# Performance work log

Measured on AMD Instinct MI355X. Metric: run time of the kernel, lower is better.

The kernel has to match this reference:

```python
import jax, jax.numpy as jnp
import numpy as np
from jax import lax

N = 2048          # batch_size*2 (two views)
DIM_IN = 1024     # stub encoder input width
DIM_FEAT = 2048
DIM = 128
C = 1000          # num_classes
Q = 8             # queue_size_per_cls
K_POS = 4         # select_num_pos
K_NEG = 1024      # select_num_neg
EPS = 1e-5


def setup_inputs() -> dict:
    key = jax.random.key(0)
    ks = jax.random.split(key, 12)
    img = jax.random.normal(ks[0], (N, DIM_IN), dtype=jnp.float32)
    labels = jax.random.randint(ks[1], (N,), 0, C)
    # buffers
    ql = jax.random.normal(ks[2], (DIM, Q * C), dtype=jnp.float32)
    queue_list = ql / jnp.linalg.norm(ql, axis=0, keepdims=True)
    queue_ptr = jnp.zeros((C,), dtype=jnp.int32)
    pos_index = jnp.asarray(np.arange(Q * C).reshape(C, Q))
    cols = np.arange(Q * (C - 1))
    # skip class-i block: indices >= Q*i shift up by Q
    neg_index = jnp.asarray(cols[None, :] + Q * ((cols[None, :] // Q) >= np.arange(C)[:, None]))
    # params (stub encoder + mlp head + classifier)
    s = 0.02
    enc_W = s * jax.random.normal(ks[3], (DIM_IN, DIM_FEAT), dtype=jnp.float32)
    enc_b = jnp.zeros((DIM_FEAT,), dtype=jnp.float32)
    mlp_W1 = s * jax.random.normal(ks[4], (DIM_FEAT, DIM_FEAT), dtype=jnp.float32)
    mlp_b1 = jnp.zeros((DIM_FEAT,), dtype=jnp.float32)
    bn_gamma = jnp.ones((DIM_FEAT,), dtype=jnp.float32)
    bn_beta = jnp.zeros((DIM_FEAT,), dtype=jnp.float32)
    mlp_W2 = s * jax.random.normal(ks[5], (DIM_FEAT, DIM), dtype=jnp.float32)
    mlp_b2 = jnp.zeros((DIM,), dtype=jnp.float32)
    lin_W = s * jax.random.normal(ks[6], (DIM_FEAT, C), dtype=jnp.float32)
    lin_b = jnp.zeros((C,), dtype=jnp.float32)
    return dict(img=img, labels=labels, queue_list=queue_list, queue_ptr=queue_ptr,
                pos_index=pos_index, neg_index=neg_index,
                enc_W=enc_W, enc_b=enc_b, mlp_W1=mlp_W1, mlp_b1=mlp_b1,
                bn_gamma=bn_gamma, bn_beta=bn_beta, mlp_W2=mlp_W2, mlp_b2=mlp_b2,
                lin_W=lin_W, lin_b=lin_b)


def _offdiag_idx(n):
    # idx[i,j] = j + (j >= i): gather columns of an [n,n] matrix skipping the diagonal
    cols = jnp.arange(n - 1)
    return cols[None, :] + (cols[None, :] >= jnp.arange(n)[:, None]).astype(cols.dtype)


def reference(img, labels, queue_list, queue_ptr, pos_index, neg_index,
              enc_W, enc_b, mlp_W1, mlp_b1, bn_gamma, bn_beta,
              mlp_W2, mlp_b2, lin_W, lin_b):
    # encoder (stub) -> mid_feat
    mid = img @ enc_W + enc_b                                  # [N, DIM_FEAT]
    # mlp: Linear -> BatchNorm1d (training stats) -> ReLU -> Linear
    h = mid @ mlp_W1 + mlp_b1
    mu = jnp.mean(h, axis=0)
    var = jnp.var(h, axis=0)
    h = (h - mu) * lax.rsqrt(var + EPS) * bn_gamma + bn_beta
    h = jax.nn.relu(h)
    feat = h @ mlp_W2 + mlp_b2
    feat = feat / jnp.linalg.norm(feat, axis=1, keepdims=True)  # [N, DIM]
    logit_cls = mid @ lin_W + lin_b                             # [N, C]

    # queue similarities (queue is detached in the original)
    ql = lax.stop_gradient(queue_list)
    sim_q = feat @ ql                                           # [N, Q*C]
    sim_pos = jnp.take_along_axis(sim_q, pos_index[labels], axis=1)   # [N, Q]
    sim_neg = jnp.take_along_axis(sim_q, neg_index[labels], axis=1)   # [N, Q*(C-1)]
    pos_sel = -lax.top_k(-sim_pos, K_POS)[0]     # hardest (smallest) positives
    neg_sel = lax.top_k(sim_neg, K_NEG)[0]       # hardest (largest) negatives

    # in-batch similarities with diagonal removed
    sim_b = feat @ feat.T                                       # [N, N]
    off = _offdiag_idx(sim_b.shape[0])
    sim_b_off = jnp.take_along_axis(sim_b, off, axis=1)         # [N, N-1]
    sim_con = jnp.concatenate([sim_b_off, pos_sel, neg_sel], axis=1)

    lab_b = (labels[:, None] == labels[None, :]).astype(jnp.float32)
    lab_off = jnp.take_along_axis(lab_b, off, axis=1)
    labels_con = jnp.concatenate([lab_off, jnp.ones_like(pos_sel), jnp.zeros_like(neg_sel)], axis=1)

    # dequeue/enqueue: sequential per-sample scatter into per-class circular buffer
    feat_k = lax.stop_gradient(feat[: feat.shape[0] // 2])
    labels_k = labels[: labels.shape[0] // 2]

    def step(carry, x):
        ql_, qp_ = carry
        f, c = x
        ptr = qp_[c]
        real = c * Q + ptr
        ql_ = ql_.at[:, real].set(f)
        qp_ = qp_.at[c].set((ptr + 1) % Q)
        return (ql_, qp_), None

    (queue_list_new, queue_ptr_new), _ = lax.scan(step, (queue_list, queue_ptr), (feat_k, labels_k))
    return sim_con, labels_con, logit_cls, queue_list_new, queue_ptr_new
```

## Files before the change

### kernel.cpp

```cpp
#include <hip/hip_runtime.h>
#include <cstdint>
#include <cstddef>

#define NB      2048
#define DIN     1024
#define DF      2048
#define DM      128
#define NCLS    1000
#define QQ      8
#define QC      8000
#define QCP     8064
#define NLP     1024
#define CONW    3075
#define FSPLIT  8
#define NBUCK   8192

using float4v = __attribute__((ext_vector_type(4))) float;
using bf16x8  = __attribute__((ext_vector_type(8))) __bf16;

#define GLB_AS __attribute__((address_space(1)))
#define LDS_AS __attribute__((address_space(3)))

__device__ __forceinline__ unsigned short f2bf(float f) {
  unsigned int u = __float_as_uint(f);
  u += 0x7fffu + ((u >> 16) & 1u);
  return (unsigned short)(u >> 16);
}
__device__ __forceinline__ float bf2f(unsigned short u) {
  return __uint_as_float(((unsigned int)u) << 16);
}

__device__ __forceinline__ bf16x8 ld_frag8(const unsigned short* p) {
  union { uint4 u; bf16x8 b; } cv;
  cv.u = *(const uint4*)p;
  return cv.b;
}

__device__ __forceinline__ void gload_lds16(const unsigned short* g, unsigned short* l) {
  __builtin_amdgcn_global_load_lds((const GLB_AS unsigned int*)g,
                                   (LDS_AS unsigned int*)l, 16, 0, 0);
}

__global__ void conv_bf16_kernel(const float* __restrict__ in, unsigned short* __restrict__ out, int n) {
  int idx = blockIdx.x * 256 + threadIdx.x;
  if (idx < n) out[idx] = f2bf(in[idx]);
}

struct TDescs {
  const float* src[5];
  unsigned short* dst[5];
  int K[5], N[5], nx[5], ky[5];
};
__global__ void transpose_all_kernel(TDescs d) {
  const int mid = blockIdx.y;
  const int nx = d.nx[mid];
  const int kb32 = blockIdx.x / nx, nb32 = blockIdx.x % nx;
  if (kb32 >= d.ky[mid]) return;
  const float* src = d.src[mid];
  unsigned short* dst = d.dst[mid];
  const int K = d.K[mid], N = d.N[mid];
  const int nb = nb32 * 32, kb = kb32 * 32;
  __shared__ float tile[32][33];
  int tx = threadIdx.x, ty = threadIdx.y;
#pragma unroll
  for (int r = 0; r < 32; r += 8) {
    int k = kb + ty + r, n = nb + tx;
    tile[ty + r][tx] = (n < N) ? src[(size_t)k * N + n] : 0.f;
  }
  __syncthreads();
#pragma unroll
  for (int r = 0; r < 32; r += 8) {
    int n = nb + ty + r, k = kb + tx;
    dst[(size_t)n * K + k] = f2bf(tile[tx][ty + r]);
  }
}

template<int OUT_MODE, bool HAS_BIAS, bool BN_STATS>
__global__ __launch_bounds__(256) void gemm_bt_kernel(
    const unsigned short* __restrict__ A,
    const unsigned short* __restrict__ Bt,
    const float* __restrict__ bias,
    const float* __restrict__ bias2,
    void* __restrict__ Cout,
    void* __restrict__ Cout2,
    int lda, int klen, int ldc, int n_store,
    float* __restrict__ ps, float* __restrict__ ps2)
{
  __shared__ __align__(16) unsigned short As[2][128][64];
  __shared__ __align__(16) unsigned short Bs[2][128][64];
  const int m0 = blockIdx.y * 128, n0 = blockIdx.x * 128;
  const int z  = blockIdx.z;
  const int tid = threadIdx.x;
  const int lane = tid & 63, w = tid >> 6;
  const int wm = (w >> 1) * 64, wn = (w & 1) * 64;
  const int lrow = lane & 15, lq = lane >> 4;
  const int r7 = lrow & 7;

  const unsigned short* Abase = A  + (size_t)m0 * lda + z * klen;
  const unsigned short* Bbase = Bt + (size_t)n0 * lda + z * klen;

  int cc[4]; size_t goff[4];
#pragma unroll
  for (int q = 0; q < 4; ++q) {
    int c = tid + 256 * q;
    int row = c >> 3;
    int ucol = (c & 7) ^ (row & 7);
    cc[q] = c;
    goff[q] = (size_t)row * lda + ucol * 8;
  }

  float4v acc[4][4];
#pragma unroll
  for (int i = 0; i < 4; ++i)
#pragma unroll
    for (int j = 0; j < 4; ++j)
      acc[i][j] = (float4v){0.f, 0.f, 0.f, 0.f};

  auto stage = [&](int buf, int k0) {
#pragma unroll
    for (int q = 0; q < 4; ++q)
      gload_lds16(Abase + goff[q] + k0, &As[buf][0][0] + cc[q] * 8);
#pragma unroll
    for (int q = 0; q < 4; ++q)
      gload_lds16(Bbase + goff[q] + k0, &Bs[buf][0][0] + cc[q] * 8);
  };

  const int NKT = klen / 64;
  stage(0, 0);
  for (int t = 0; t < NKT; ++t) {
    __syncthreads();
    if (t + 1 < NKT) stage((t + 1) & 1, (t + 1) * 64);
    const int b = t & 1;
#pragma unroll
    for (int kk = 0; kk < 2; ++kk) {
      bf16x8 af[4], bfr[4];
#pragma unroll
      for (int i = 0; i < 4; ++i)
        af[i]  = ld_frag8(&As[b][wm + i * 16 + lrow][(((kk << 2) + lq) ^ r7) << 3]);
#pragma unroll
      for (int j = 0; j < 4; ++j)
        bfr[j] = ld_frag8(&Bs[b][wn + j * 16 + lrow][(((kk << 2) + lq) ^ r7) << 3]);
#pragma unroll
      for (int i = 0; i < 4; ++i)
#pragma unroll
        for (int j = 0; j < 4; ++j)
          acc[i][j] = __builtin_amdgcn_mfma_f32_16x16x32_bf16(af[i], bfr[j], acc[i][j], 0, 0, 0);
    }
  }

  const bool is2nd = (OUT_MODE == 3 && n0 >= DF) || (OUT_MODE == 4 && n0 >= QCP);
  const bool do_bn = BN_STATS && !is2nd;

  float* cs  = (float*)&As[0][0][0];
  float* cs2 = cs + 128;
  if (do_bn) {
    __syncthreads();
    if (tid < 256) cs[tid] = 0.f;
    __syncthreads();
  }

  float*          outf  = (float*)Cout          + (size_t)z * NB * ldc;
  unsigned short* outh  = (unsigned short*)Cout + (size_t)z * NB * ldc;
  float*          outf2 = (float*)Cout2;

#pragma unroll
  for (int j = 0; j < 4; ++j) {
    int gcol = n0 + wn + j * 16 + lrow;
    float bv = 0.f;
    if (OUT_MODE == 3) {
      if (!is2nd) bv = bias[gcol];
      else if (gcol - DF < NCLS) bv = bias2[gcol - DF];
    } else if (HAS_BIAS && gcol < n_store) bv = bias[gcol];
    float sj = 0.f, s2j = 0.f;
#pragma unroll
    for (int i = 0; i < 4; ++i) {
#pragma unroll
      for (int r = 0; r < 4; ++r) {
        int grow = m0 + wm + i * 16 + lq * 4 + r;
        float val = acc[i][j][r] + bv;
        if (do_bn) { sj += val; s2j += val * val; }
        if (OUT_MODE == 0) {
          if (gcol < n_store) outf[(size_t)grow * ldc + gcol] = val;
        } else if (OUT_MODE == 1) {
          if (gcol < n_store) outh[(size_t)grow * ldc + gcol] = f2bf(val);
        } else if (OUT_MODE == 3) {
          if (!is2nd) outh[(size_t)grow * DF + gcol] = f2bf(val);
          else if (gcol - DF < NCLS) outf2[(size_t)grow * NCLS + (gcol - DF)] = val;
        } else if (OUT_MODE == 4) {
          if (!is2nd) { if (gcol < QC) outh[(size_t)grow * QC + gcol] = f2bf(val); }
          else {
            int gc2 = gcol - QCP;
            if (gc2 != grow) outf2[(size_t)grow * CONW + gc2 - (gc2 > grow)] = val;
          }
        }
      }
    }
    if (do_bn) {
      atomicAdd(&cs [wn + j * 16 + lrow], sj);
      atomicAdd(&cs2[wn + j * 16 + lrow], s2j);
    }
  }
  if (do_bn) {
    __syncthreads();
    if (tid < 128) {
      ps [(size_t)blockIdx.y * DF + n0 + tid] = cs[tid];
      ps2[(size_t)blockIdx.y * DF + n0 + tid] = cs2[tid];
    }
  }
}

__global__ void bn_finish_kernel(const float* __restrict__ ps, const float* __restrict__ ps2,
                                 const float* __restrict__ gamma, const float* __restrict__ beta,
                                 float* __restrict__ scale, float* __restrict__ bias) {
  int j = blockIdx.x * 256 + threadIdx.x;
  float s = 0.f, s2 = 0.f;
  for (int b = 0; b < 16; ++b) { s += ps[b * DF + j]; s2 += ps2[b * DF + j]; }
  float mu  = s  * (1.f / NB);
  float var = s2 * (1.f / NB) - mu * mu;
  float sc = gamma[j] * rsqrtf(var + 1e-5f);
  scale[j] = sc;
  bias[j]  = beta[j] - mu * sc;
}

__global__ void bn_apply_kernel(const unsigned short* __restrict__ h, const float* __restrict__ scale,
                                const float* __restrict__ bias, unsigned short* __restrict__ hb) {
  int base = (blockIdx.x * 256 + threadIdx.x) * 8;
  int j = base & (DF - 1);
  uint4 u = *(const uint4*)(h + base);
  unsigned int uu[4] = {u.x, u.y, u.z, u.w};
  unsigned int rr[4];
#pragma unroll
  for (int e = 0; e < 4; ++e) {
    int col = j + 2 * e;
    float lo = bf2f((unsigned short)(uu[e] & 0xffffu));
    float hi = bf2f((unsigned short)(uu[e] >> 16));
    lo = fmaxf(lo * scale[col] + bias[col], 0.f);
    hi = fmaxf(hi * scale[col + 1] + bias[col + 1], 0.f);
    rr[e] = (unsigned int)f2bf(lo) | ((unsigned int)f2bf(hi) << 16);
  }
  uint4 o; o.x = rr[0]; o.y = rr[1]; o.z = rr[2]; o.w = rr[3];
  *(uint4*)(hb + base) = o;
}

__global__ void feat_reduce_norm_kernel(const float* __restrict__ part, const float* __restrict__ b2,
                                        float* __restrict__ fo, unsigned short* __restrict__ fb) {
  int row = blockIdx.x, t = threadIdx.x;
  float v0 = b2[t], v1 = b2[64 + t];
#pragma unroll
  for (int s = 0; s < FSPLIT; ++s) {
    const float* p = part + (size_t)s * NB * DM + (size_t)row * DM;
    v0 += p[t]; v1 += p[64 + t];
  }
  float ss = v0 * v0 + v1 * v1;
#pragma unroll
  for (int o = 32; o > 0; o >>= 1) ss += __shfl_xor(ss, o);
  float inv = rsqrtf(ss);
  v0 *= inv; v1 *= inv;
  fo[row * DM + t] = v0;       fo[row * DM + 64 + t] = v1;
  fb[row * DM + t] = f2bf(v0); fb[row * DM + 64 + t] = f2bf(v1);
}

__global__ __launch_bounds__(256) void topk_kernel(const unsigned short* __restrict__ sim_qb,
                                                   const int* __restrict__ labels,
                                                   float* __restrict__ out_simcon) {
  __shared__ unsigned int hist[NBUCK];
  __shared__ float sbuf[1024];
  __shared__ unsigned int wtot[4];
  __shared__ int s_tb;

  const int row = blockIdx.x;
  const int c = labels[row];
  const int t = threadIdx.x;
  const int w = t >> 6, lane = t & 63;

  uint4* h4 = (uint4*)hist;
  uint4 z4; z4.x = z4.y = z4.z = z4.w = 0u;
#pragma unroll
  for (int i = 0; i < 8; ++i) h4[t + 256 * i] = z4;

  float vals[32];
  float pvals[QQ];
  const unsigned short* rp = sim_qb + (size_t)row * QC;
#pragma unroll
  for (int j = 0; j < 4; ++j) {
    const int cls = j * 256 + t;
    uint4 u4 = *(const uint4*)(rp + j * 2048 + t * 8);
    const unsigned int uu[4] = {u4.x, u4.y, u4.z, u4.w};
    const bool masked = (cls >= NCLS) || (cls == c);
#pragma unroll
    for (int e = 0; e < 4; ++e) {
      float lo = bf2f((unsigned short)(uu[e] & 0xffffu));
      float hi = bf2f((unsigned short)(uu[e] >> 16));
      if (cls == c) { pvals[2 * e] = lo; pvals[2 * e + 1] = hi; }
      vals[j * 8 + 2 * e]     = masked ? -4.f : lo;
      vals[j * 8 + 2 * e + 1] = masked ? -4.f : hi;
    }
  }
  __syncthreads();

#pragma unroll
  for (int i = 0; i < 32; ++i) {
    float v = vals[i];
    if (v > -3.f) {
      int b = (int)((v + 1.0f) * 4096.0f);
      b = min(max(b, 0), NBUCK - 1);
      atomicAdd(&hist[b], 1u);
    }
  }
  __syncthreads();

  unsigned int cnt[32];
#pragma unroll
  for (int k = 0; k < 8; ++k) {
    uint4 u = h4[t * 8 + k];
    cnt[4 * k] = u.x; cnt[4 * k + 1] = u.y; cnt[4 * k + 2] = u.z; cnt[4 * k + 3] = u.w;
  }
  unsigned int chunktot = 0;
#pragma unroll
  for (int i = 0; i < 32; ++i) chunktot += cnt[i];

  unsigned int s = chunktot;
#pragma unroll
  for (int off = 1; off < 64; off <<= 1) {
    unsigned int v = __shfl_down(s, off);
    if (lane + off < 64) s += v;
  }
  if (lane == 0) wtot[w] = s;
  __syncthreads();
  unsigned int wsfx = 0;
#pragma unroll
  for (int ww = 0; ww < 4; ++ww) if (ww > w) wsfx += wtot[ww];
  unsigned int S = wsfx + s - chunktot;

  unsigned int ofsv[32];
#pragma unroll
  for (int i = 31; i >= 0; --i) {
    unsigned int cb = cnt[i];
    ofsv[i] = S;
    unsigned int Sincl = S + cb;
    if (S < 1024u && Sincl >= 1024u) s_tb = t * 32 + i;
    S = Sincl;
  }
#pragma unroll
  for (int k = 0; k < 8; ++k) {
    uint4 u;
    u.x = ofsv[4 * k]; u.y = ofsv[4 * k + 1]; u.z = ofsv[4 * k + 2]; u.w = ofsv[4 * k + 3];
    h4[t * 8 + k] = u;
  }
  __syncthreads();

  const int tb = s_tb;
#pragma unroll
  for (int i = 0; i < 32; ++i) {
    float v = vals[i];
    if (v > -3.f) {
      int b = (int)((v + 1.0f) * 4096.0f);
      b = min(max(b, 0), NBUCK - 1);
      if (b >= tb) {
        unsigned int p = atomicAdd(&hist[b], 1u);
        if (p < 1024u) sbuf[p] = v;
      }
    }
  }
  __syncthreads();

  float* orow = out_simcon + (size_t)row * CONW;
  for (int idx = t; idx < 1024; idx += 256) orow[2051 + idx] = sbuf[idx];
  if (t == (c & 255) && (c >> 8) < 4 && (c >> 8) * 256 + t == c) {
    for (int a2 = 1; a2 < QQ; ++a2) {
      float key = pvals[a2]; int b2 = a2 - 1;
      while (b2 >= 0 && pvals[b2] > key) { pvals[b2 + 1] = pvals[b2]; --b2; }
      pvals[b2 + 1] = key;
    }
#pragma unroll
    for (int s2 = 0; s2 < 4; ++s2) orow[2047 + s2] = pvals[s2];
  }
}

__global__ void labels_con_kernel(const int* __restrict__ labels, float* __restrict__ out_lab) {
  int i = blockIdx.x;
  int li = labels[i];
  for (int j = threadIdx.x; j < CONW; j += 256) {
    float v;
    if (j < NB - 1)      v = (labels[j + (j >= i)] == li) ? 1.f : 0.f;
    else if (j < NB + 3) v = 1.f;
    else                 v = 0.f;
    out_lab[(size_t)i * CONW + j] = v;
  }
}

__global__ void queue_scan_kernel(const int* __restrict__ labels, const int* __restrict__ qptr_in,
                                  int* __restrict__ writer, float* __restrict__ qptr_out) {
  __shared__ int wloc[QQ];
  const int c = blockIdx.x;
  const int lane = threadIdx.x;
  if (lane < QQ) wloc[lane] = -1;
  __syncthreads();
  const int p0 = qptr_in[c];
  int cnt = 0;
#pragma unroll
  for (int t = 0; t < (NB / 2) / 64; ++t) {
    int i = t * 64 + lane;
    bool pred = (labels[i] == c);
    unsigned long long mask = __ballot(pred);
    if (pred) {
      int rank = __popcll(mask & ((1ull << lane) - 1ull));
      int slot = (p0 + cnt + rank) & (QQ - 1);
      atomicMax(&wloc[slot], i);
    }
    cnt += __popcll(mask);
  }
  __syncthreads();
  if (lane < QQ) writer[c * QQ + lane] = wloc[lane];
  if (lane == 0) qptr_out[c] = (float)((p0 + cnt) & (QQ - 1));
}

__global__ void queue_write_kernel(const int* __restrict__ writer, const float* __restrict__ feat,
                                   const float* __restrict__ qin, float* __restrict__ qout) {
  int idx = blockIdx.x * 256 + threadIdx.x;
  int col = idx % QC;
  int d   = idx / QC;
  int wsrc = writer[col];
  float v = (wsrc >= 0) ? feat[(size_t)wsrc * DM + d] : qin[idx];
  qout[idx] = v;
}

extern "C" void kernel_launch(void* const* d_in, const int* in_sizes, int n_in,
                              void* d_out, int out_size, void* d_ws, size_t ws_size,
                              hipStream_t stream) {
  const float* img     = (const float*)d_in[0];
  const int*   labels  = (const int*)  d_in[1];
  const float* queue_l = (const float*)d_in[2];
  const int*   queue_p = (const int*)  d_in[3];
  const float* enc_W   = (const float*)d_in[6];
  const float* enc_b   = (const float*)d_in[7];
  const float* W1      = (const float*)d_in[8];
  const float* b1      = (const float*)d_in[9];
  const float* gamma   = (const float*)d_in[10];
  const float* beta    = (const float*)d_in[11];
  const float* W2      = (const float*)d_in[12];
  const float* b2      = (const float*)d_in[13];
  const float* linW    = (const float*)d_in[14];
  const float* linb    = (const float*)d_in[15];

  float* out        = (float*)d_out;
  float* out_simcon = out;
  float* out_labcon = out + (size_t)NB * CONW;
  float* out_logit  = out + (size_t)2 * NB * CONW;
  float* out_qlist  = out_logit + (size_t)NB * NCLS;
  float* out_qptr   = out_qlist + (size_t)DM * QC;

  char* wsp = (char*)d_ws;
  size_t off = 0;
  auto alloc = [&](size_t bytes) -> void* {
    void* p = wsp + off;
    off += (bytes + 255) & ~(size_t)255;
    return p;
  };
  unsigned short* img_bf  = (unsigned short*)alloc((size_t)NB * DIN * 2);
  unsigned short* encWt   = (unsigned short*)alloc((size_t)DF * DIN * 2);
  unsigned short* W1t     = (unsigned short*)alloc((size_t)DF * DF * 2);
  unsigned short* linWt   = (unsigned short*)alloc((size_t)NLP * DF * 2);
  unsigned short* W2t     = (unsigned short*)alloc((size_t)DM * DF * 2);
  unsigned short* qlt     = (unsigned short*)alloc((size_t)QCP * DM * 2);
  unsigned short* feat_bf = (unsigned short*)alloc((size_t)NB * DM * 2);
  unsigned short* mid_bf  = (unsigned short*)alloc((size_t)NB * DF * 2);
  unsigned short* h_pbf   = (unsigned short*)alloc((size_t)NB * DF * 2);
  unsigned short* h_bf    = (unsigned short*)alloc((size_t)NB * DF * 2);
  float*          part_s  = (float*)alloc((size_t)16 * DF * 4);
  float*          part_s2 = (float*)alloc((size_t)16 * DF * 4);
  float*          bn_sc   = (float*)alloc((size_t)DF * 4);
  float*          bn_bi   = (float*)alloc((size_t)DF * 4);
  float*          feat_part=(float*)alloc((size_t)FSPLIT * NB * DM * 4);
  float*          feat_f  = (float*)alloc((size_t)NB * DM * 4);
  unsigned short* sim_qb  = (unsigned short*)alloc((size_t)NB * QC * 2 + 512);
  int*            writer  = (int*)alloc((size_t)QC * 4);

  dim3 blk256(256);
  dim3 tblk(32, 8);

  conv_bf16_kernel<<<dim3((NB * DIN) / 256), blk256, 0, stream>>>(img, img_bf, NB * DIN);
  TDescs td;
  td.src[0] = enc_W;  td.dst[0] = encWt; td.K[0] = DIN; td.N[0] = DF;   td.nx[0] = DF / 32;   td.ky[0] = DIN / 32;
  td.src[1] = W1;     td.dst[1] = W1t;   td.K[1] = DF;  td.N[1] = DF;   td.nx[1] = DF / 32;   td.ky[1] = DF / 32;
  td.src[2] = W2;     td.dst[2] = W2t;   td.K[2] = DF;  td.N[2] = DM;   td.nx[2] = DM / 32;   td.ky[2] = DF / 32;
  td.src[3] = linW;   td.dst[3] = linWt; td.K[3] = DF;  td.N[3] = NCLS; td.nx[3] = NLP / 32;  td.ky[3] = DF / 32;
  td.src[4] = queue_l;td.dst[4] = qlt;   td.K[4] = DM;  td.N[4] = QC;   td.nx[4] = QCP / 32;  td.ky[4] = DM / 32;
  transpose_all_kernel<<<dim3(4096, 5), tblk, 0, stream>>>(td);

  gemm_bt_kernel<1, true, false><<<dim3(DF / 128, NB / 128), blk256, 0, stream>>>(
      img_bf, encWt, enc_b, nullptr, mid_bf, nullptr, DIN, DIN, DF, DF, nullptr, nullptr);

  gemm_bt_kernel<3, true, true><<<dim3((DF + NLP) / 128, NB / 128), blk256, 0, stream>>>(
      mid_bf, W1t, b1, linb, h_pbf, out_logit, DF, DF, DF, DF, part_s, part_s2);

  bn_finish_kernel<<<dim3(DF / 256), blk256, 0, stream>>>(part_s, part_s2, gamma, beta, bn_sc, bn_bi);
  bn_apply_kernel<<<dim3((NB * DF) / 2048), blk256, 0, stream>>>(h_pbf, bn_sc, bn_bi, h_bf);

  gemm_bt_kernel<0, false, false><<<dim3(DM / 128, NB / 128, FSPLIT), blk256, 0, stream>>>(
      h_bf, W2t, nullptr, nullptr, feat_part, nullptr, DF, DF / FSPLIT, DM, DM, nullptr, nullptr);

  feat_reduce_norm_kernel<<<dim3(NB), dim3(64), 0, stream>>>(feat_part, b2, feat_f, feat_bf);

  gemm_bt_kernel<4, false, false><<<dim3((QCP + NB) / 128, NB / 128), blk256, 0, stream>>>(
      feat_bf, qlt, nullptr, nullptr, sim_qb, out_simcon, DM, DM, QC, QC, nullptr, nullptr);

  topk_kernel<<<dim3(NB), blk256, 0, stream>>>(sim_qb, labels, out_simcon);

  labels_con_kernel<<<dim3(NB), blk256, 0, stream>>>(labels, out_labcon);

  queue_scan_kernel<<<dim3(NCLS), dim3(64), 0, stream>>>(labels, queue_p, writer, out_qptr);
  queue_write_kernel<<<dim3((DM * QC) / 256), blk256, 0, stream>>>(writer, feat_f, queue_l, out_qlist);
}
```

Before: 311.0 us.

## Load GEMM B fragments directly from global into registers, bypassing LDS

The B operand is no longer staged through shared memory. Each wave loads its B fragments straight from global memory into registers, double-buffered across k-tiles, while A keeps its LDS double buffer, and the main loop is unrolled by two. This halves LDS use and LDS traffic, which could raise occupancy. In exchange, B rows are read repeatedly by the waves that share them with less coalescing, register pressure rises, and the unconditional stage of tile t+1 assumes NKT is even.

```diff
diff --git a/kernel.cpp b/kernel.cpp
--- a/kernel.cpp
+++ b/kernel.cpp
@@ -87,7 +87,6 @@
     float* __restrict__ ps, float* __restrict__ ps2)
 {
   __shared__ __align__(16) unsigned short As[2][128][64];
-  __shared__ __align__(16) unsigned short Bs[2][128][64];
   const int m0 = blockIdx.y * 128, n0 = blockIdx.x * 128;
   const int z  = blockIdx.z;
   const int tid = threadIdx.x;
@@ -97,7 +96,7 @@
   const int r7 = lrow & 7;
 
   const unsigned short* Abase = A  + (size_t)m0 * lda + z * klen;
-  const unsigned short* Bbase = Bt + (size_t)n0 * lda + z * klen;
+  const unsigned short* Bw = Bt + (size_t)(n0 + wn + lrow) * lda + z * klen + lq * 8;
 
   int cc[4]; size_t goff[4];
 #pragma unroll
@@ -116,36 +115,45 @@
     for (int j = 0; j < 4; ++j)
       acc[i][j] = (float4v){0.f, 0.f, 0.f, 0.f};
 
-  auto stage = [&](int buf, int k0) {
+  auto stageA = [&](int buf, int k0) {
 #pragma unroll
     for (int q = 0; q < 4; ++q)
       gload_lds16(Abase + goff[q] + k0, &As[buf][0][0] + cc[q] * 8);
-#pragma unroll
-    for (int q = 0; q < 4; ++q)
-      gload_lds16(Bbase + goff[q] + k0, &Bs[buf][0][0] + cc[q] * 8);
   };
+  auto loadB = [&](int t, bf16x8 (&dst)[8]) {
+#pragma unroll
+    for (int kk = 0; kk < 2; ++kk)
+#pragma unroll
+      for (int j = 0; j < 4; ++j)
+        dst[kk * 4 + j] = ld_frag8(Bw + (size_t)(j * 16) * lda + t * 64 + kk * 32);
+  };
+  auto compute = [&](int b, const bf16x8 (&bfr)[8]) {
+#pragma unroll
+    for (int kk = 0; kk < 2; ++kk) {
+      bf16x8 af[4];
+#pragma unroll
+      for (int i = 0; i < 4; ++i)
+        af[i] = ld_frag8(&As[b][wm + i * 16 + lrow][(((kk << 2) + lq) ^ r7) << 3]);
+#pragma unroll
+      for (int i = 0; i < 4; ++i)
+#pragma unroll
+        for (int j = 0; j < 4; ++j)
+          acc[i][j] = __builtin_amdgcn_mfma_f32_16x16x32_bf16(af[i], bfr[kk * 4 + j], acc[i][j], 0, 0, 0);
+    }
+  };
 
   const int NKT = klen / 64;
-  stage(0, 0);
-  for (int t = 0; t < NKT; ++t) {
+  bf16x8 bA[8], bB[8];
+  stageA(0, 0);
+  loadB(0, bA);
+  for (int t = 0; t < NKT; t += 2) {
     __syncthreads();
-    if (t + 1 < NKT) stage((t + 1) & 1, (t + 1) * 64);
-    const int b = t & 1;
-#pragma unroll
-    for (int kk = 0; kk < 2; ++kk) {
-      bf16x8 af[4], bfr[4];
-#pragma unroll
-      for (int i = 0; i < 4; ++i)
-        af[i]  = ld_frag8(&As[b][wm + i * 16 + lrow][(((kk << 2) + lq) ^ r7) << 3]);
-#pragma unroll
-      for (int j = 0; j < 4; ++j)
-        bfr[j] = ld_frag8(&Bs[b][wn + j * 16 + lrow][(((kk << 2) + lq) ^ r7) << 3]);
-#pragma unroll
-      for (int i = 0; i < 4; ++i)
-#pragma unroll
-        for (int j = 0; j < 4; ++j)
-          acc[i][j] = __builtin_amdgcn_mfma_f32_16x16x32_bf16(af[i], bfr[j], acc[i][j], 0, 0, 0);
-    }
+    stageA(1, (t + 1) * 64);
+    loadB(t + 1, bB);
+    compute(0, bA);
+    __syncthreads();
+    if (t + 2 < NKT) { stageA(0, (t + 2) * 64); loadB(t + 2, bA); }
+    compute(1, bB);
   }
 
   const bool is2nd = (OUT_MODE == 3 && n0 >= DF) || (OUT_MODE == 4 && n0 >= QCP);
```

New measurement: 368.2 us. 1.18x slower.

## Fuse small kernels and remap GEMM workgroups to cut launches

Applied to the files above, without the earlier changes.

Folds the fp32-to-bf16 image conversion into the weight transpose kernel and merges BN finish into the first MLP GEMM through a last-block atomic counter. Also merges the labels_con writes into the top-k kernel and the queue scan and queue write into one per-class kernel, removing four launches. Adds a workgroup-ID swizzle to the GEMMs so neighbouring workgroups land on the same XCD for cache locality. The risks are the threadfence and counter ordering in the last-block reduction and a serial BN reduction tail in one block.

```diff
diff --git a/kernel.cpp b/kernel.cpp
--- a/kernel.cpp
+++ b/kernel.cpp
@@ -14,6 +14,7 @@
 #define CONW    3075
 #define FSPLIT  8
 #define NBUCK   8192
+#define NBN     256
 
 using float4v = __attribute__((ext_vector_type(4))) float;
 using bf16x8  = __attribute__((ext_vector_type(8))) __bf16;
@@ -41,18 +42,28 @@
                                    (LDS_AS unsigned int*)l, 16, 0, 0);
 }
 
-__global__ void conv_bf16_kernel(const float* __restrict__ in, unsigned short* __restrict__ out, int n) {
-  int idx = blockIdx.x * 256 + threadIdx.x;
-  if (idx < n) out[idx] = f2bf(in[idx]);
-}
-
 struct TDescs {
-  const float* src[5];
-  unsigned short* dst[5];
-  int K[5], N[5], nx[5], ky[5];
+  const float* src[6];
+  unsigned short* dst[6];
+  int K[6], N[6], nx[6], ky[6];
 };
-__global__ void transpose_all_kernel(TDescs d) {
+__global__ void prep_kernel(TDescs d, unsigned int* __restrict__ bn_cnt) {
   const int mid = blockIdx.y;
+  const int tid = threadIdx.y * 32 + threadIdx.x;
+  if (mid == 5) {
+    if (blockIdx.x == 0 && tid == 0) *bn_cnt = 0u;
+    if (blockIdx.x < (NB * DIN) / 1024) {
+      const float* src = d.src[5];
+      unsigned short* dst = d.dst[5];
+      int base = blockIdx.x * 1024 + tid * 4;
+      float4 f = *(const float4*)(src + base);
+      unsigned int lo = (unsigned int)f2bf(f.x) | ((unsigned int)f2bf(f.y) << 16);
+      unsigned int hi = (unsigned int)f2bf(f.z) | ((unsigned int)f2bf(f.w) << 16);
+      uint2 o; o.x = lo; o.y = hi;
+      *(uint2*)(dst + base) = o;
+    }
+    return;
+  }
   const int nx = d.nx[mid];
   const int kb32 = blockIdx.x / nx, nb32 = blockIdx.x % nx;
   if (kb32 >= d.ky[mid]) return;
@@ -84,11 +95,18 @@
     void* __restrict__ Cout,
     void* __restrict__ Cout2,
     int lda, int klen, int ldc, int n_store,
-    float* __restrict__ ps, float* __restrict__ ps2)
+    float* __restrict__ ps, float* __restrict__ ps2,
+    const float* __restrict__ gamma, const float* __restrict__ beta,
+    float* __restrict__ bnsc, float* __restrict__ bnbi,
+    unsigned int* __restrict__ bn_cnt)
 {
   __shared__ __align__(16) unsigned short As[2][128][64];
   __shared__ __align__(16) unsigned short Bs[2][128][64];
-  const int m0 = blockIdx.y * 128, n0 = blockIdx.x * 128;
+  const int nwg = gridDim.x * gridDim.y;
+  int wid = blockIdx.y * gridDim.x + blockIdx.x;
+  wid = (wid & 7) * (nwg >> 3) + (wid >> 3);
+  const int bx = wid % gridDim.x, by = wid / gridDim.x;
+  const int m0 = by * 128, n0 = bx * 128;
   const int z  = blockIdx.z;
   const int tid = threadIdx.x;
   const int lane = tid & 63, w = tid >> 6;
@@ -203,23 +221,27 @@
   if (do_bn) {
     __syncthreads();
     if (tid < 128) {
-      ps [(size_t)blockIdx.y * DF + n0 + tid] = cs[tid];
-      ps2[(size_t)blockIdx.y * DF + n0 + tid] = cs2[tid];
-    }
-  }
-}
-
-__global__ void bn_finish_kernel(const float* __restrict__ ps, const float* __restrict__ ps2,
-                                 const float* __restrict__ gamma, const float* __restrict__ beta,
-                                 float* __restrict__ scale, float* __restrict__ bias) {
-  int j = blockIdx.x * 256 + threadIdx.x;
-  float s = 0.f, s2 = 0.f;
-  for (int b = 0; b < 16; ++b) { s += ps[b * DF + j]; s2 += ps2[b * DF + j]; }
-  float mu  = s  * (1.f / NB);
-  float var = s2 * (1.f / NB) - mu * mu;
-  float sc = gamma[j] * rsqrtf(var + 1e-5f);
-  scale[j] = sc;
-  bias[j]  = beta[j] - mu * sc;
+      ps [(size_t)by * DF + n0 + tid] = cs[tid];
+      ps2[(size_t)by * DF + n0 + tid] = cs2[tid];
+    }
+    __threadfence();
+    __syncthreads();
+    __shared__ unsigned int s_old;
+    if (tid == 0) s_old = atomicAdd(bn_cnt, 1u);
+    __syncthreads();
+    if (s_old == NBN - 1) {
+      for (int jj = tid; jj < DF; jj += 256) {
+        float s = 0.f, s2 = 0.f;
+#pragma unroll
+        for (int b2 = 0; b2 < 16; ++b2) { s += ps[b2 * DF + jj]; s2 += ps2[b2 * DF + jj]; }
+        float mu  = s  * (1.f / NB);
+        float var = s2 * (1.f / NB) - mu * mu;
+        float sc = gamma[jj] * rsqrtf(var + 1e-5f);
+        bnsc[jj] = sc;
+        bnbi[jj] = beta[jj] - mu * sc;
+      }
+    }
+  }
 }
 
 __global__ void bn_apply_kernel(const unsigned short* __restrict__ h, const float* __restrict__ scale,
@@ -262,7 +284,8 @@
 
 __global__ __launch_bounds__(256) void topk_kernel(const unsigned short* __restrict__ sim_qb,
                                                    const int* __restrict__ labels,
-                                                   float* __restrict__ out_simcon) {
+                                                   float* __restrict__ out_simcon,
+                                                   float* __restrict__ out_labcon) {
   __shared__ unsigned int hist[NBUCK];
   __shared__ float sbuf[1024];
   __shared__ unsigned int wtot[4];
@@ -375,54 +398,55 @@
 #pragma unroll
     for (int s2 = 0; s2 < 4; ++s2) orow[2047 + s2] = pvals[s2];
   }
-}
-
-__global__ void labels_con_kernel(const int* __restrict__ labels, float* __restrict__ out_lab) {
-  int i = blockIdx.x;
-  int li = labels[i];
-  for (int j = threadIdx.x; j < CONW; j += 256) {
+
+  float* lrow = out_labcon + (size_t)row * CONW;
+  for (int j = t; j < CONW; j += 256) {
     float v;
-    if (j < NB - 1)      v = (labels[j + (j >= i)] == li) ? 1.f : 0.f;
+    if (j < NB - 1)      v = (labels[j + (j >= row)] == c) ? 1.f : 0.f;
     else if (j < NB + 3) v = 1.f;
     else                 v = 0.f;
-    out_lab[(size_t)i * CONW + j] = v;
-  }
-}
-
-__global__ void queue_scan_kernel(const int* __restrict__ labels, const int* __restrict__ qptr_in,
-                                  int* __restrict__ writer, float* __restrict__ qptr_out) {
+    lrow[j] = v;
+  }
+}
+
+__global__ void queue_update_kernel(const int* __restrict__ labels, const int* __restrict__ qptr_in,
+                                    const float* __restrict__ feat, const float* __restrict__ qin,
+                                    float* __restrict__ qout, float* __restrict__ qptr_out) {
   __shared__ int wloc[QQ];
   const int c = blockIdx.x;
-  const int lane = threadIdx.x;
-  if (lane < QQ) wloc[lane] = -1;
+  const int t = threadIdx.x;
+  const int lane = t & 63;
+  if (t < QQ) wloc[t] = -1;
   __syncthreads();
   const int p0 = qptr_in[c];
-  int cnt = 0;
-#pragma unroll
-  for (int t = 0; t < (NB / 2) / 64; ++t) {
-    int i = t * 64 + lane;
-    bool pred = (labels[i] == c);
-    unsigned long long mask = __ballot(pred);
-    if (pred) {
-      int rank = __popcll(mask & ((1ull << lane) - 1ull));
-      int slot = (p0 + cnt + rank) & (QQ - 1);
-      atomicMax(&wloc[slot], i);
-    }
-    cnt += __popcll(mask);
-  }
-  __syncthreads();
-  if (lane < QQ) writer[c * QQ + lane] = wloc[lane];
-  if (lane == 0) qptr_out[c] = (float)((p0 + cnt) & (QQ - 1));
-}
-
-__global__ void queue_write_kernel(const int* __restrict__ writer, const float* __restrict__ feat,
-                                   const float* __restrict__ qin, float* __restrict__ qout) {
-  int idx = blockIdx.x * 256 + threadIdx.x;
-  int col = idx % QC;
-  int d   = idx / QC;
-  int wsrc = writer[col];
-  float v = (wsrc >= 0) ? feat[(size_t)wsrc * DM + d] : qin[idx];
-  qout[idx] = v;
+  if (t < 64) {
+    int cnt = 0;
+#pragma unroll
+    for (int it = 0; it < (NB / 2) / 64; ++it) {
+      int i = it * 64 + lane;
+      bool pred = (labels[i] == c);
+      unsigned long long mask = __ballot(pred);
+      if (pred) {
+        int rank = __popcll(mask & ((1ull << lane) - 1ull));
+        int slot = (p0 + cnt + rank) & (QQ - 1);
+        atomicMax(&wloc[slot], i);
+      }
+      cnt += __popcll(mask);
+    }
+    if (lane == 0) qptr_out[c] = (float)((p0 + cnt) & (QQ - 1));
+  }
+  __syncthreads();
+  const int d = t >> 1, half = t & 1;
+  const size_t rowbase = (size_t)d * QC + c * QQ + half * 4;
+  float4 v = *(const float4*)(qin + rowbase);
+  float vv[4] = {v.x, v.y, v.z, v.w};
+#pragma unroll
+  for (int s = 0; s < 4; ++s) {
+    int wsrc = wloc[half * 4 + s];
+    if (wsrc >= 0) vv[s] = feat[(size_t)wsrc * DM + d];
+  }
+  float4 o; o.x = vv[0]; o.y = vv[1]; o.z = vv[2]; o.w = vv[3];
+  *(float4*)(qout + rowbase) = o;
 }
 
 extern "C" void kernel_launch(void* const* d_in, const int* in_sizes, int n_in,
@@ -474,41 +498,42 @@
   float*          feat_part=(float*)alloc((size_t)FSPLIT * NB * DM * 4);
   float*          feat_f  = (float*)alloc((size_t)NB * DM * 4);
   unsigned short* sim_qb  = (unsigned short*)alloc((size_t)NB * QC * 2 + 512);
-  int*            writer  = (int*)alloc((size_t)QC * 4);
+  unsigned int*   bn_cnt  = (unsigned int*)alloc(256);
 
   dim3 blk256(256);
   dim3 tblk(32, 8);
 
-  conv_bf16_kernel<<<dim3((NB * DIN) / 256), blk256, 0, stream>>>(img, img_bf, NB * DIN);
   TDescs td;
   td.src[0] = enc_W;  td.dst[0] = encWt; td.K[0] = DIN; td.N[0] = DF;   td.nx[0] = DF / 32;   td.ky[0] = DIN / 32;
   td.src[1] = W1;     td.dst[1] = W1t;   td.K[1] = DF;  td.N[1] = DF;   td.nx[1] = DF / 32;   td.ky[1] = DF / 32;
   td.src[2] = W2;     td.dst[2] = W2t;   td.K[2] = DF;  td.N[2] = DM;   td.nx[2] = DM / 32;   td.ky[2] = DF / 32;
   td.src[3] = linW;   td.dst[3] = linWt; td.K[3] = DF;  td.N[3] = NCLS; td.nx[3] = NLP / 32;  td.ky[3] = DF / 32;
   td.src[4] = queue_l;td.dst[4] = qlt;   td.K[4] = DM;  td.N[4] = QC;   td.nx[4] = QCP / 32;  td.ky[4] = DM / 32;
-  transpose_all_kernel<<<dim3(4096, 5), tblk, 0, stream>>>(td);
+  td.src[5] = img;    td.dst[5] = img_bf;td.K[5] = 0;   td.N[5] = 0;    td.nx[5] = 1;         td.ky[5] = 0;
+  prep_kernel<<<dim3(4096, 6), tblk, 0, stream>>>(td, bn_cnt);
 
   gemm_bt_kernel<1, true, false><<<dim3(DF / 128, NB / 128), blk256, 0, stream>>>(
-      img_bf, encWt, enc_b, nullptr, mid_bf, nullptr, DIN, DIN, DF, DF, nullptr, nullptr);
+      img_bf, encWt, enc_b, nullptr, mid_bf, nullptr, DIN, DIN, DF, DF, nullptr, nullptr,
+      nullptr, nullptr, nullptr, nullptr, nullptr);
 
   gemm_bt_kernel<3, true, true><<<dim3((DF + NLP) / 128, NB / 128), blk256, 0, stream>>>(
-      mid_bf, W1t, b1, linb, h_pbf, out_logit, DF, DF, DF, DF, part_s, part_s2);
-
-  bn_finish_kernel<<<dim3(DF / 256), blk256, 0, stream>>>(part_s, part_s2, gamma, beta, bn_sc, bn_bi);
+      mid_bf, W1t, b1, linb, h_pbf, out_logit, DF, DF, DF, DF, part_s, part_s2,
+      gamma, beta, bn_sc, bn_bi, bn_cnt);
+
   bn_apply_kernel<<<dim3((NB * DF) / 2048), blk256, 0, stream>>>(h_pbf, bn_sc, bn_bi, h_bf);
 
   gemm_bt_kernel<0, false, false><<<dim3(DM / 128, NB / 128, FSPLIT), blk256, 0, stream>>>(
-      h_bf, W2t, nullptr, nullptr, feat_part, nullptr, DF, DF / FSPLIT, DM, DM, nullptr, nullptr);
+      h_bf, W2t, nullptr, nullptr, feat_part, nullptr, DF, DF / FSPLIT, DM, DM, nullptr, nullptr,
+      nullptr, nullptr, nullptr, nullptr, nullptr);
 
   feat_reduce_norm_kernel<<<dim3(NB), dim3(64), 0, stream>>>(feat_part, b2, feat_f, feat_bf);
 
   gemm_bt_kernel<4, false, false><<<dim3((QCP + NB) / 128, NB / 128), blk256, 0, stream>>>(
-      feat_bf, qlt, nullptr, nullptr, sim_qb, out_simcon, DM, DM, QC, QC, nullptr, nullptr);
-
-  topk_kernel<<<dim3(NB), blk256, 0, stream>>>(sim_qb, labels, out_simcon);
-
-  labels_con_kernel<<<dim3(NB), blk256, 0, stream>>>(labels, out_labcon);
-
-  queue_scan_kernel<<<dim3(NCLS), dim3(64), 0, stream>>>(labels, queue_p, writer, out_qptr);
-  queue_write_kernel<<<dim3((DM * QC) / 256), blk256, 0, stream>>>(writer, feat_f, queue_l, out_qlist);
-}
+      feat_bf, qlt, nullptr, nullptr, sim_qb, out_simcon, DM, DM, QC, QC, nullptr, nullptr,
+      nullptr, nullptr, nullptr, nullptr, nullptr);
+
+  topk_kernel<<<dim3(NB), blk256, 0, stream>>>(sim_qb, labels, out_simcon, out_labcon);
+
+  queue_update_kernel<<<dim3(NCLS), blk256, 0, stream>>>(labels, queue_p, feat_f, queue_l,
+                                                         out_qlist, out_qptr);
+}
```

Result: slower. 331.9 us (+6.7%).
